# Kernel optimization log

Measured on AMD Instinct MI355X. Metric: run time of the kernel, lower is better.

The kernel has to match this reference:

```python
import jax, jax.numpy as jnp
import numpy as np

B, L, D, H = 4, 2048, 1024, 16
DH = D // H  # 64
MASK_VALUE = -1000000.0
EPS = 1e-12


def setup_inputs() -> dict:
    key = jax.random.key(0)
    ks = jax.random.split(key, 7)
    s = 1.0 / np.sqrt(D)
    x = jax.random.normal(ks[0], (B, L, D), dtype=jnp.float32)
    Wq = jax.random.uniform(ks[1], (D, H * DH), jnp.float32, -s, s)
    Wk = jax.random.uniform(ks[2], (D, H * DH), jnp.float32, -s, s)
    Wv = jax.random.uniform(ks[3], (D, H * DH), jnp.float32, -s, s)
    Wo = jax.random.uniform(ks[4], (H * DH, D), jnp.float32, -s, s)
    gamma = jnp.ones((D,), jnp.float32)
    beta = jnp.zeros((D,), jnp.float32)
    # causal mask: True positions are masked (query m cannot attend to key n > m)
    attn_mask = jnp.triu(jnp.ones((L, L), dtype=bool), k=1)
    return {"x": x, "Wq": Wq, "Wk": Wk, "Wv": Wv, "Wo": Wo,
            "gamma": gamma, "beta": beta, "attn_mask": attn_mask}


def _layernorm(y, gamma, beta):
    mu = jnp.mean(y, axis=-1, keepdims=True)
    var = jnp.mean(jnp.square(y - mu), axis=-1, keepdims=True)
    return (y - mu) * jax.lax.rsqrt(var + EPS) * gamma + beta


def reference(x, Wq, Wk, Wv, Wo, gamma, beta, attn_mask):
    scale = 1.0 / np.sqrt(DH)
    # projections, reshape to heads: B L (H D) -> B H L D
    q = (x @ Wq).reshape(B, L, H, DH).transpose(0, 2, 1, 3)
    k = (x @ Wk).reshape(B, L, H, DH).transpose(0, 2, 1, 3)
    v = (x @ Wv).reshape(B, L, H, DH).transpose(0, 2, 1, 3)
    scores = jnp.einsum('bhmd,bhnd->bhmn', q, k) * scale
    scores = jnp.where(attn_mask, MASK_VALUE, scores)
    probs = jax.nn.softmax(scores, axis=-1)
    z = jnp.einsum('bhmn,bhnd->bhmd', probs, v)
    z = z.transpose(0, 2, 1, 3).reshape(B, L, H * DH)
    out = jax.nn.relu(z @ Wo)
    return _layernorm(out + x, gamma, beta)
```

## Files before the change

kernel.cpp:

```cpp
#include <hip/hip_runtime.h>
#include <math.h>

#define B_ 4
#define L_ 2048
#define D_ 1024
#define H_ 16
#define DH_ 64
#define QKV_N 3072

typedef unsigned short ushort_t;
typedef unsigned int uint_t;
using bf16x8 = __attribute__((ext_vector_type(8))) short;
using f32x4  = __attribute__((ext_vector_type(4))) float;

__device__ __forceinline__ ushort_t f2bf(float f) {
    union { float f; unsigned int u; } v; v.f = f;
    unsigned int u = v.u;
    unsigned int rnd = ((u >> 16) & 1u) + 0x7fffu;
    return (ushort_t)((u + rnd) >> 16);
}

__device__ __forceinline__ float bf2f(ushort_t u) {
    union { unsigned int u; float f; } v;
    v.u = ((unsigned int)u) << 16;
    return v.f;
}

__device__ __forceinline__ void glds16(const void* g, void* l) {
    __builtin_amdgcn_global_load_lds(
        (const __attribute__((address_space(1))) unsigned int*)g,
        (__attribute__((address_space(3))) unsigned int*)l, 16, 0, 0);
}

__global__ __launch_bounds__(256) void prep(const float* __restrict__ Wq,
                                            const float* __restrict__ Wk,
                                            const float* __restrict__ Wv,
                                            const float* __restrict__ Wo,
                                            const float* __restrict__ x,
                                            ushort_t* __restrict__ wcat,
                                            ushort_t* __restrict__ wto,
                                            ushort_t* __restrict__ xb) {
    const int t = threadIdx.x;
    if (blockIdx.z == 4) {
        const int bid = blockIdx.y * 16 + blockIdx.x;
        const int base = bid * 32768 + t * 4;
        #pragma unroll
        for (int it = 0; it < 32; ++it) {
            float4 v = *(const float4*)(x + base + it * 1024);
            ushort4 o;
            o.x = f2bf(v.x); o.y = f2bf(v.y); o.z = f2bf(v.z); o.w = f2bf(v.w);
            *(ushort4*)(xb + base + it * 1024) = o;
        }
        return;
    }
    __shared__ ushort_t tile[64][65];
    const int widx = blockIdx.z;
    const float* W = (widx == 0) ? Wq : (widx == 1) ? Wk : (widx == 2) ? Wv : Wo;
    ushort_t* dst = (widx < 3) ? (wcat + (size_t)widx * 1024 * 1024) : wto;
    const int j = t & 63, i0 = t >> 6;
    const int kbase = blockIdx.y * 64, nbase = blockIdx.x * 64;
    #pragma unroll
    for (int it = 0; it < 16; ++it) {
        int i = it * 4 + i0;
        tile[i][j] = f2bf(W[(size_t)(kbase + i) * 1024 + nbase + j]);
    }
    __syncthreads();
    #pragma unroll
    for (int it = 0; it < 16; ++it) {
        int nn = it * 4 + i0;
        dst[(size_t)(nbase + nn) * 1024 + kbase + j] = tile[j][nn];
    }
}

__global__ __launch_bounds__(512) void gemm8p(const ushort_t* __restrict__ A,
                                              const ushort_t* __restrict__ Wt,
                                              ushort_t* __restrict__ Cbf,
                                              const ushort_t* __restrict__ resid,
                                              ushort_t* __restrict__ vt,
                                              int M, int N, int K, int fuse) {
    __shared__ ushort_t lds[49152];
    const int t = threadIdx.x;
    const int w = t >> 6, ln = t & 63;
    const int l15 = ln & 15, quad = ln >> 4;
    const int wrow = w >> 1, wcol = w & 1;

    int bx = blockIdx.x, by = blockIdx.y;
    {
        int nwg = gridDim.x * gridDim.y;
        if ((nwg & 7) == 0) {
            int flat = by * gridDim.x + bx;
            int nid = (flat & 7) * (nwg >> 3) + (flat >> 3);
            by = nid / gridDim.x;
            bx = nid - by * gridDim.x;
        }
    }
    const int bm = by * 256, bn = bx * 128;

    const ushort_t* Agp[2];
    const ushort_t* Bgp;
    #pragma unroll
    for (int j = 0; j < 2; ++j) {
        int r = j * 128 + (t >> 2);
        int c = (t & 3) ^ ((r >> 1) & 3);
        Agp[j] = A + (size_t)(bm + r) * K + c * 8;
    }
    {
        int r = t >> 2;
        int c = (t & 3) ^ ((r >> 1) & 3);
        Bgp = Wt + (size_t)(bn + r) * K + c * 8;
    }

    const int swz8 = (quad ^ ((l15 >> 1) & 3)) * 8;
    int aoff[4], boff[4];
    #pragma unroll
    for (int mf = 0; mf < 4; ++mf)
        aoff[mf] = (wrow * 64 + mf * 16 + l15) * 32 + swz8;
    #pragma unroll
    for (int nf = 0; nf < 4; ++nf)
        boff[nf] = (wcol * 64 + nf * 16 + l15) * 32 + swz8;

    f32x4 acc[4][4] = {};
    const int NT = K >> 6;

#define ABASE(BUF, KH) ((BUF) * 24576 + (KH) * 12288)
#define BBASE(BUF, KH) (ABASE(BUF, KH) + 8192)

#define STAGE(BUF, KH, KT) do {                                             \
        glds16(Agp[0] + (KT) * 64 + (KH) * 32, &lds[ABASE(BUF, KH) + t * 8]);\
        glds16(Agp[1] + (KT) * 64 + (KH) * 32,                              \
               &lds[ABASE(BUF, KH) + 4096 + t * 8]);                        \
        glds16(Bgp + (KT) * 64 + (KH) * 32, &lds[BBASE(BUF, KH) + t * 8]);  \
    } while (0)

#define VM6 asm volatile("s_waitcnt vmcnt(6)" ::: "memory")
#define VM3 asm volatile("s_waitcnt vmcnt(3)" ::: "memory")
#define VM0 asm volatile("s_waitcnt vmcnt(0)" ::: "memory")
#define NOVM ((void)0)

#define PHASE(BUF, KH, STAGEC, VMW) do {                                    \
        bf16x8 af_[4], bf_[4];                                              \
        _Pragma("unroll")                                                   \
        for (int m_ = 0; m_ < 4; ++m_)                                      \
            af_[m_] = *(const bf16x8*)&lds[ABASE(BUF, KH) + aoff[m_]];      \
        _Pragma("unroll")                                                   \
        for (int n_ = 0; n_ < 4; ++n_)                                      \
            bf_[n_] = *(const bf16x8*)&lds[BBASE(BUF, KH) + boff[n_]];      \
        STAGEC;                                                             \
        VMW;                                                                \
        __builtin_amdgcn_s_barrier();                                       \
        asm volatile("s_waitcnt lgkmcnt(0)" ::: "memory");                  \
        __builtin_amdgcn_s_setprio(1);                                      \
        _Pragma("unroll")                                                   \
        for (int m_ = 0; m_ < 4; ++m_)                                      \
            _Pragma("unroll")                                               \
            for (int n_ = 0; n_ < 4; ++n_)                                  \
                acc[m_][n_] = __builtin_amdgcn_mfma_f32_16x16x32_bf16(      \
                    af_[m_], bf_[n_], acc[m_][n_], 0, 0, 0);                \
        __builtin_amdgcn_s_setprio(0);                                      \
        __builtin_amdgcn_s_barrier();                                       \
    } while (0)

    STAGE(0, 0, 0);
    STAGE(0, 1, 0);
    STAGE(1, 0, 1);
    VM6;
    __builtin_amdgcn_s_barrier();

    for (int it = 0; it < (NT >> 1) - 1; ++it) {
        const int kt1 = 2 * it + 1, kt2 = 2 * it + 2, kt3 = 2 * it + 3;
        PHASE(0, 0, STAGE(1, 1, kt1), VM6);
        PHASE(0, 1, STAGE(0, 0, kt2), VM6);
        PHASE(1, 0, STAGE(0, 1, kt2), VM6);
        PHASE(1, 1, STAGE(1, 0, kt3), VM6);
    }

    PHASE(0, 0, STAGE(1, 1, NT - 1), VM6);
    PHASE(0, 1, NOVM, VM3);
    PHASE(1, 0, NOVM, VM0);
    PHASE(1, 1, NOVM, NOVM);

#undef PHASE
#undef STAGE
#undef ABASE
#undef BBASE

    if (vt && bn >= 2048) {
        #pragma unroll
        for (int mf = 0; mf < 4; ++mf) {
            #pragma unroll
            for (int nf = 0; nf < 4; ++nf) {
                #pragma unroll
                for (int reg = 0; reg < 4; ++reg) {
                    int row = bm + wrow * 64 + mf * 16 + quad * 4 + reg;
                    int col = bn + wcol * 64 + nf * 16 + l15 - 2048;
                    int bb = row >> 11, tok = row & 2047;
                    int h = col >> 6, d = col & 63;
                    int tg = tok & 63;
                    int sc = (tg & 15) * 4 + (tg >> 4);
                    size_t addr = ((size_t)((bb * 16 + h) * 64 + d) << 11)
                                + (tok & ~63) + sc;
                    vt[addr] = f2bf(acc[mf][nf][reg]);
                }
            }
        }
    } else {
        #pragma unroll
        for (int mf = 0; mf < 4; ++mf) {
            #pragma unroll
            for (int nf = 0; nf < 4; ++nf) {
                #pragma unroll
                for (int reg = 0; reg < 4; ++reg) {
                    int row = bm + wrow * 64 + mf * 16 + quad * 4 + reg;
                    int col = bn + wcol * 64 + nf * 16 + l15;
                    size_t idx = (size_t)row * N + col;
                    float v = acc[mf][nf][reg];
                    if (fuse) v = fmaxf(v, 0.f) + bf2f(resid[idx]);
                    Cbf[idx] = f2bf(v);
                }
            }
        }
    }
}

__global__ __launch_bounds__(256) void gemm_mfma(const ushort_t* __restrict__ A,
                                                 const ushort_t* __restrict__ Wt,
                                                 ushort_t* __restrict__ Cbf,
                                                 const ushort_t* __restrict__ resid,
                                                 ushort_t* __restrict__ vt,
                                                 int M, int N, int K, int fuse) {
    __shared__ ushort_t As[128 * 64];
    __shared__ ushort_t Bs[128 * 64];
    const int t = threadIdx.x;
    const int w = t >> 6, ln = t & 63;
    const int l15 = ln & 15, quad = ln >> 4;
    const int bm = blockIdx.y * 128, bn = blockIdx.x * 128;
    const int wm = (w & 1) * 64, wn = (w >> 1) * 64;

    const ushort_t* Ap[4];
    const ushort_t* Bp[4];
    #pragma unroll
    for (int j = 0; j < 4; ++j) {
        const int i = t + j * 256;
        const int r = i >> 3;
        const int qg = (i & 7) ^ (r & 7);
        Ap[j] = A  + (size_t)(bm + r) * K + qg * 8;
        Bp[j] = Wt + (size_t)(bn + r) * K + qg * 8;
    }

    f32x4 acc[4][4] = {};

    for (int k0 = 0; k0 < K; k0 += 64) {
        __syncthreads();
        #pragma unroll
        for (int j = 0; j < 4; ++j) {
            glds16(Ap[j] + k0, &As[(t + j * 256) * 8]);
            glds16(Bp[j] + k0, &Bs[(t + j * 256) * 8]);
        }
        __syncthreads();

        #pragma unroll
        for (int kw = 0; kw < 2; ++kw) {
            bf16x8 af[4], bfr[4];
            #pragma unroll
            for (int im = 0; im < 4; ++im) {
                int row = wm + im * 16 + l15;
                int phys = (kw * 4 + quad) ^ (row & 7);
                af[im] = *(const bf16x8*)&As[row * 64 + phys * 8];
            }
            #pragma unroll
            for (int in = 0; in < 4; ++in) {
                int row = wn + in * 16 + l15;
                int phys = (kw * 4 + quad) ^ (row & 7);
                bfr[in] = *(const bf16x8*)&Bs[row * 64 + phys * 8];
            }
            #pragma unroll
            for (int im = 0; im < 4; ++im)
                #pragma unroll
                for (int in = 0; in < 4; ++in)
                    acc[im][in] = __builtin_amdgcn_mfma_f32_16x16x32_bf16(
                        af[im], bfr[in], acc[im][in], 0, 0, 0);
        }
    }

    if (vt && bn >= 2048) {
        #pragma unroll
        for (int im = 0; im < 4; ++im) {
            #pragma unroll
            for (int in = 0; in < 4; ++in) {
                #pragma unroll
                for (int reg = 0; reg < 4; ++reg) {
                    int row = bm + wm + im * 16 + quad * 4 + reg;
                    int col = bn + wn + in * 16 + l15 - 2048;
                    int bb = row >> 11, tok = row & 2047;
                    int h = col >> 6, d = col & 63;
                    int tg = tok & 63;
                    int sc = (tg & 15) * 4 + (tg >> 4);
                    size_t addr = ((size_t)((bb * 16 + h) * 64 + d) << 11)
                                + (tok & ~63) + sc;
                    vt[addr] = f2bf(acc[im][in][reg]);
                }
            }
        }
    } else {
        #pragma unroll
        for (int im = 0; im < 4; ++im) {
            #pragma unroll
            for (int in = 0; in < 4; ++in) {
                #pragma unroll
                for (int reg = 0; reg < 4; ++reg) {
                    int row = bm + wm + im * 16 + quad * 4 + reg;
                    int col = bn + wn + in * 16 + l15;
                    size_t idx = (size_t)row * N + col;
                    float v = acc[im][in][reg];
                    if (fuse) v = fmaxf(v, 0.f) + bf2f(resid[idx]);
                    Cbf[idx] = f2bf(v);
                }
            }
        }
    }
}

__global__ __launch_bounds__(256) void attn_mfma(const ushort_t* __restrict__ qkv,
                                                 const ushort_t* __restrict__ Vt,
                                                 ushort_t* __restrict__ Zb) {
    __shared__ ushort_t Ks[128 * 64];
    __shared__ ushort_t Vs[64 * 128];
    __shared__ ushort_t Ps[4][32 * 72];
    const int t = threadIdx.x, w = t >> 6, ln = t & 63;
    const int l15 = ln & 15, quad = ln >> 4;
    const int bh = blockIdx.x;
    const int b = bh >> 4, h = bh & 15;
    const int Qt = 15 - blockIdx.y;

    bf16x8 ones;
    #pragma unroll
    for (int i = 0; i < 8; ++i) ones[i] = (short)0x3f80;

    int kkey[4], kq[4], vd[4], vcq[4];
    #pragma unroll
    for (int j = 0; j < 4; ++j) {
        int i = t + j * 256;
        kkey[j] = i >> 3;
        kq[j]   = (i & 7) ^ (kkey[j] & 7);
        vd[j]   = i >> 4;
        int cqp = i & 15;
        vcq[j]  = (cqp & 8) | ((cqp & 7) ^ (vd[j] & 7));
    }
    const ushort_t* Kgb = qkv + 1024 + (size_t)b * L_ * QKV_N + h * DH_;
    const ushort_t* Vgb = Vt + (size_t)((b * H_ + h) * DH_) * L_;

    bf16x8 qf[2][2];
    #pragma unroll
    for (int mt = 0; mt < 2; ++mt) {
        const ushort_t* qrow =
            qkv + (size_t)(b * L_ + Qt * 128 + w * 32 + mt * 16 + l15) * QKV_N + h * DH_;
        qf[mt][0] = *(const bf16x8*)(qrow + quad * 8);
        qf[mt][1] = *(const bf16x8*)(qrow + 32 + quad * 8);
    }

    f32x4 acc_o[2][4] = {};
    f32x4 l_acc[2] = {};

    const float c2 = 0.18033688f;

    for (int kt = 0; kt <= Qt; ++kt) {
        __syncthreads();
        #pragma unroll
        for (int j = 0; j < 4; ++j) {
            glds16(Kgb + (size_t)(kt * 128 + kkey[j]) * QKV_N + kq[j] * 8,
                   &Ks[(t + j * 256) * 8]);
            glds16(Vgb + (size_t)vd[j] * L_ + kt * 128 + vcq[j] * 8,
                   &Vs[(t + j * 256) * 8]);
        }
        __syncthreads();

        const bool masked = (kt == Qt);

        #pragma unroll
        for (int ph = 0; ph < 2; ++ph) {
            if (masked && ph && w < 2) continue;

            f32x4 acc_s[2][4] = {};
            __builtin_amdgcn_s_setprio(1);
            #pragma unroll
            for (int in = 0; in < 4; ++in) {
                const int key = ph * 64 + in * 16 + l15;
                #pragma unroll
                for (int ks = 0; ks < 2; ++ks) {
                    int phys = (ks * 4 + quad) ^ (key & 7);
                    bf16x8 kf = *(const bf16x8*)&Ks[key * 64 + phys * 8];
                    acc_s[0][in] = __builtin_amdgcn_mfma_f32_16x16x32_bf16(
                        qf[0][ks], kf, acc_s[0][in], 0, 0, 0);
                    acc_s[1][in] = __builtin_amdgcn_mfma_f32_16x16x32_bf16(
                        qf[1][ks], kf, acc_s[1][in], 0, 0, 0);
                }
            }
            __builtin_amdgcn_s_setprio(0);

            #pragma unroll
            for (int mt = 0; mt < 2; ++mt) {
                #pragma unroll
                for (int reg = 0; reg < 4; ++reg) {
                    const int row = mt * 16 + quad * 4 + reg;
                    float pv[4];
                    #pragma unroll
                    for (int in = 0; in < 4; ++in) {
                        float s2 = fmaf(acc_s[mt][in][reg], c2, -2.0f);
                        if (masked) {
                            int col = kt * 128 + ph * 64 + in * 16 + l15;
                            int qg  = Qt * 128 + w * 32 + row;
                            s2 = (col > qg) ? -100000.0f : s2;
                        }
                        pv[in] = __builtin_amdgcn_exp2f(s2);
                    }
                    uint_t u01 = __builtin_amdgcn_perm(
                        __float_as_uint(pv[1]), __float_as_uint(pv[0]), 0x07060302u);
                    uint_t u23 = __builtin_amdgcn_perm(
                        __float_as_uint(pv[3]), __float_as_uint(pv[2]), 0x07060302u);
                    uint2* dst = (uint2*)&Ps[w][row * 72 + l15 * 4];
                    *dst = make_uint2(u01, u23);
                }
            }

            __builtin_amdgcn_s_setprio(1);
            #pragma unroll
            for (int ks = 0; ks < 2; ++ks) {
                bf16x8 pf0 = *(const bf16x8*)&Ps[w][(l15) * 72 + ks * 32 + quad * 8];
                bf16x8 pf1 = *(const bf16x8*)&Ps[w][(16 + l15) * 72 + ks * 32 + quad * 8];
                #pragma unroll
                for (int in = 0; in < 4; ++in) {
                    const int d = in * 16 + l15;
                    int physv = ph * 8 + (((ks * 4 + quad) ^ (d & 7)));
                    bf16x8 vf = *(const bf16x8*)&Vs[d * 128 + physv * 8];
                    acc_o[0][in] = __builtin_amdgcn_mfma_f32_16x16x32_bf16(
                        vf, pf0, acc_o[0][in], 0, 0, 0);
                    acc_o[1][in] = __builtin_amdgcn_mfma_f32_16x16x32_bf16(
                        vf, pf1, acc_o[1][in], 0, 0, 0);
                }
                l_acc[0] = __builtin_amdgcn_mfma_f32_16x16x32_bf16(ones, pf0, l_acc[0], 0, 0, 0);
                l_acc[1] = __builtin_amdgcn_mfma_f32_16x16x32_bf16(ones, pf1, l_acc[1], 0, 0, 0);
            }
            __builtin_amdgcn_s_setprio(0);
        }
    }

    #pragma unroll
    for (int mt = 0; mt < 2; ++mt) {
        const float inv = 1.0f / l_acc[mt][0];
        const int row = b * L_ + Qt * 128 + w * 32 + mt * 16 + l15;
        #pragma unroll
        for (int in = 0; in < 4; ++in) {
            const int dbase = h * DH_ + in * 16 + quad * 4;
            f32x4 a = acc_o[mt][in];
            ushort4 o;
            o.x = f2bf(a[0] * inv); o.y = f2bf(a[1] * inv);
            o.z = f2bf(a[2] * inv); o.w = f2bf(a[3] * inv);
            *(ushort4*)(Zb + (size_t)row * D_ + dbase) = o;
        }
    }
}

__global__ __launch_bounds__(256) void ln_kernel(const ushort_t* __restrict__ Y,
                                                 const float* __restrict__ gamma,
                                                 const float* __restrict__ beta,
                                                 float* __restrict__ out) {
    const int row = blockIdx.x * 4 + (threadIdx.x >> 6);
    const int t = threadIdx.x & 63;
    const ushort_t* y = Y + (size_t)row * D_;

    float v[16];
    #pragma unroll
    for (int s = 0; s < 4; ++s) {
        ushort4 u = *(const ushort4*)(y + s * 256 + t * 4);
        v[s * 4 + 0] = bf2f(u.x);
        v[s * 4 + 1] = bf2f(u.y);
        v[s * 4 + 2] = bf2f(u.z);
        v[s * 4 + 3] = bf2f(u.w);
    }

    float sum = 0.f;
    #pragma unroll
    for (int i = 0; i < 16; ++i) sum += v[i];
    #pragma unroll
    for (int k = 1; k < 64; k <<= 1) sum += __shfl_xor(sum, k, 64);
    const float mu = sum * (1.f / (float)D_);

    float var = 0.f;
    #pragma unroll
    for (int i = 0; i < 16; ++i) {
        float d = v[i] - mu;
        var += d * d;
    }
    #pragma unroll
    for (int k = 1; k < 64; k <<= 1) var += __shfl_xor(var, k, 64);
    const float rstd = rsqrtf(var * (1.f / (float)D_) + 1e-12f);

    #pragma unroll
    for (int s = 0; s < 4; ++s) {
        const int col = s * 256 + t * 4;
        float4 g  = *(const float4*)(gamma + col);
        float4 bb = *(const float4*)(beta + col);
        float4 o;
        o.x = (v[s * 4 + 0] - mu) * rstd * g.x + bb.x;
        o.y = (v[s * 4 + 1] - mu) * rstd * g.y + bb.y;
        o.z = (v[s * 4 + 2] - mu) * rstd * g.z + bb.z;
        o.w = (v[s * 4 + 3] - mu) * rstd * g.w + bb.w;
        *(float4*)(out + (size_t)row * D_ + col) = o;
    }
}

extern "C" void kernel_launch(void* const* d_in, const int* in_sizes, int n_in,
                              void* d_out, int out_size, void* d_ws, size_t ws_size,
                              hipStream_t stream) {
    const float* x     = (const float*)d_in[0];
    const float* Wq    = (const float*)d_in[1];
    const float* Wk    = (const float*)d_in[2];
    const float* Wv    = (const float*)d_in[3];
    const float* Wo    = (const float*)d_in[4];
    const float* gamma = (const float*)d_in[5];
    const float* beta  = (const float*)d_in[6];
    float* out = (float*)d_out;

    char* ws = (char*)d_ws;
    ushort_t* x_bf = (ushort_t*)(ws);
    ushort_t* wcat = (ushort_t*)(ws + (16u  << 20));
    ushort_t* wto  = (ushort_t*)(ws + (22u  << 20));
    ushort_t* qkv  = (ushort_t*)(ws + (24u  << 20));
    ushort_t* vt   = (ushort_t*)(ws + (72u  << 20));
    ushort_t* z_bf = (ushort_t*)(ws + (88u  << 20));
    ushort_t* y_bf = (ushort_t*)(ws + (104u << 20));

    const int M = B_ * L_;

    prep<<<dim3(16, 16, 5), 256, 0, stream>>>(Wq, Wk, Wv, Wo, x, wcat, wto, x_bf);

    gemm8p<<<dim3(QKV_N / 128, M / 256), 512, 0, stream>>>(
        x_bf, wcat, qkv, nullptr, vt, M, QKV_N, D_, 0);

    attn_mfma<<<dim3(B_ * H_, 16), 256, 0, stream>>>(qkv, vt, z_bf);

    gemm_mfma<<<dim3(D_ / 128, M / 128), 256, 0, stream>>>(
        z_bf, wto, y_bf, x_bf, nullptr, M, D_, D_, 1);

    ln_kernel<<<M / 4, 256, 0, stream>>>(y_bf, gamma, beta, out);
}
```

Measured before the change: 281.4 us.

## Double-buffer K/V tiles in attention with 64-key stages to overlap loads

Attention now stages K and V in two 64-key LDS buffers instead of one 128-key buffer. The loads for the next tile are issued before computing on the current one, so global-to-LDS latency can overlap the MFMA work. Each iteration needs one barrier instead of two. The trade-off is twice as many iterations and barriers per query tile, and it relies on glds16 completion being covered by the end-of-iteration sync.

```diff
diff --git a/kernel.cpp b/kernel.cpp
--- a/kernel.cpp
+++ b/kernel.cpp
@@ -323,8 +323,8 @@
 __global__ __launch_bounds__(256) void attn_mfma(const ushort_t* __restrict__ qkv,
                                                  const ushort_t* __restrict__ Vt,
                                                  ushort_t* __restrict__ Zb) {
-    __shared__ ushort_t Ks[128 * 64];
-    __shared__ ushort_t Vs[64 * 128];
+    __shared__ ushort_t Ks[2][64 * 64];
+    __shared__ ushort_t Vs[2][64 * 64];
     __shared__ ushort_t Ps[4][32 * 72];
     const int t = threadIdx.x, w = t >> 6, ln = t & 63;
     const int l15 = ln & 15, quad = ln >> 4;
@@ -336,15 +336,12 @@
     #pragma unroll
     for (int i = 0; i < 8; ++i) ones[i] = (short)0x3f80;
 
-    int kkey[4], kq[4], vd[4], vcq[4];
-    #pragma unroll
-    for (int j = 0; j < 4; ++j) {
+    int sr[2], sc[2];
+    #pragma unroll
+    for (int j = 0; j < 2; ++j) {
         int i = t + j * 256;
-        kkey[j] = i >> 3;
-        kq[j]   = (i & 7) ^ (kkey[j] & 7);
-        vd[j]   = i >> 4;
-        int cqp = i & 15;
-        vcq[j]  = (cqp & 8) | ((cqp & 7) ^ (vd[j] & 7));
+        sr[j] = i >> 3;
+        sc[j] = (i & 7) ^ (sr[j] & 7);
     }
     const ushort_t* Kgb = qkv + 1024 + (size_t)b * L_ * QKV_N + h * DH_;
     const ushort_t* Vgb = Vt + (size_t)((b * H_ + h) * DH_) * L_;
@@ -363,32 +360,37 @@
 
     const float c2 = 0.18033688f;
 
-    for (int kt = 0; kt <= Qt; ++kt) {
-        __syncthreads();
-        #pragma unroll
-        for (int j = 0; j < 4; ++j) {
-            glds16(Kgb + (size_t)(kt * 128 + kkey[j]) * QKV_N + kq[j] * 8,
-                   &Ks[(t + j * 256) * 8]);
-            glds16(Vgb + (size_t)vd[j] * L_ + kt * 128 + vcq[j] * 8,
-                   &Vs[(t + j * 256) * 8]);
-        }
-        __syncthreads();
-
-        const bool masked = (kt == Qt);
-
-        #pragma unroll
-        for (int ph = 0; ph < 2; ++ph) {
-            if (masked && ph && w < 2) continue;
-
+#define ASTAGE(BUF, KK) do {                                                \
+        glds16(Kgb + (size_t)((KK) * 64 + sr[0]) * QKV_N + sc[0] * 8,       \
+               &Ks[BUF][t * 8]);                                            \
+        glds16(Kgb + (size_t)((KK) * 64 + sr[1]) * QKV_N + sc[1] * 8,       \
+               &Ks[BUF][(t + 256) * 8]);                                    \
+        glds16(Vgb + (size_t)sr[0] * L_ + (KK) * 64 + sc[0] * 8,            \
+               &Vs[BUF][t * 8]);                                            \
+        glds16(Vgb + (size_t)sr[1] * L_ + (KK) * 64 + sc[1] * 8,            \
+               &Vs[BUF][(t + 256) * 8]);                                    \
+    } while (0)
+
+    const int last = 2 * Qt + 1;
+
+    ASTAGE(0, 0);
+    __syncthreads();
+
+    for (int kk = 0; kk <= last; ++kk) {
+        const int cur = kk & 1;
+        if (kk < last) ASTAGE(cur ^ 1, kk + 1);
+
+        const bool maskedTile = (kk >= 2 * Qt);
+        if (!(kk == last && w < 2)) {
             f32x4 acc_s[2][4] = {};
             __builtin_amdgcn_s_setprio(1);
             #pragma unroll
             for (int in = 0; in < 4; ++in) {
-                const int key = ph * 64 + in * 16 + l15;
+                const int key = in * 16 + l15;
                 #pragma unroll
                 for (int ks = 0; ks < 2; ++ks) {
                     int phys = (ks * 4 + quad) ^ (key & 7);
-                    bf16x8 kf = *(const bf16x8*)&Ks[key * 64 + phys * 8];
+                    bf16x8 kf = *(const bf16x8*)&Ks[cur][key * 64 + phys * 8];
                     acc_s[0][in] = __builtin_amdgcn_mfma_f32_16x16x32_bf16(
                         qf[0][ks], kf, acc_s[0][in], 0, 0, 0);
                     acc_s[1][in] = __builtin_amdgcn_mfma_f32_16x16x32_bf16(
@@ -406,8 +408,8 @@
                     #pragma unroll
                     for (int in = 0; in < 4; ++in) {
                         float s2 = fmaf(acc_s[mt][in][reg], c2, -2.0f);
-                        if (masked) {
-                            int col = kt * 128 + ph * 64 + in * 16 + l15;
+                        if (maskedTile) {
+                            int col = kk * 64 + in * 16 + l15;
                             int qg  = Qt * 128 + w * 32 + row;
                             s2 = (col > qg) ? -100000.0f : s2;
                         }
@@ -430,8 +432,8 @@
                 #pragma unroll
                 for (int in = 0; in < 4; ++in) {
                     const int d = in * 16 + l15;
-                    int physv = ph * 8 + (((ks * 4 + quad) ^ (d & 7)));
-                    bf16x8 vf = *(const bf16x8*)&Vs[d * 128 + physv * 8];
+                    int physv = (ks * 4 + quad) ^ (d & 7);
+                    bf16x8 vf = *(const bf16x8*)&Vs[cur][d * 64 + physv * 8];
                     acc_o[0][in] = __builtin_amdgcn_mfma_f32_16x16x32_bf16(
                         vf, pf0, acc_o[0][in], 0, 0, 0);
                     acc_o[1][in] = __builtin_amdgcn_mfma_f32_16x16x32_bf16(
@@ -442,7 +444,11 @@
             }
             __builtin_amdgcn_s_setprio(0);
         }
-    }
+
+        __syncthreads();
+    }
+
+#undef ASTAGE
 
     #pragma unroll
     for (int mt = 0; mt < 2; ++mt) {
```

Measured after the change: 287.1 us. 1.02x slower.

## Replace 4-slot GEMM LDS pipeline with 3-slot rotating ring buffer

Applied to the files above, without the earlier changes.

The GEMM k-loop drops from four 32-wide LDS slots (double buffer of two halves) to a three-slot rotating ring, keeping prefetch depth at two stages ahead. Shared memory per block falls from 96KB to 72KB, which may let more workgroups or waves reside per CU. The trade-off is one fewer in-flight stage and runtime slot-pointer rotation instead of compile-time constant LDS offsets, which may add address arithmetic and lose some latency hiding.

```diff
diff --git a/kernel.cpp b/kernel.cpp
--- a/kernel.cpp
+++ b/kernel.cpp
@@ -78,7 +78,7 @@
                                               const ushort_t* __restrict__ resid,
                                               ushort_t* __restrict__ vt,
                                               int M, int N, int K, int fuse) {
-    __shared__ ushort_t lds[49152];
+    __shared__ ushort_t lds[36864];
     const int t = threadIdx.x;
     const int w = t >> 6, ln = t & 63;
     const int l15 = ln & 15, quad = ln >> 4;
@@ -117,34 +117,29 @@
         aoff[mf] = (wrow * 64 + mf * 16 + l15) * 32 + swz8;
     #pragma unroll
     for (int nf = 0; nf < 4; ++nf)
-        boff[nf] = (wcol * 64 + nf * 16 + l15) * 32 + swz8;
+        boff[nf] = 8192 + (wcol * 64 + nf * 16 + l15) * 32 + swz8;
 
     f32x4 acc[4][4] = {};
-    const int NT = K >> 6;
-
-#define ABASE(BUF, KH) ((BUF) * 24576 + (KH) * 12288)
-#define BBASE(BUF, KH) (ABASE(BUF, KH) + 8192)
-
-#define STAGE(BUF, KH, KT) do {                                             \
-        glds16(Agp[0] + (KT) * 64 + (KH) * 32, &lds[ABASE(BUF, KH) + t * 8]);\
-        glds16(Agp[1] + (KT) * 64 + (KH) * 32,                              \
-               &lds[ABASE(BUF, KH) + 4096 + t * 8]);                        \
-        glds16(Bgp + (KT) * 64 + (KH) * 32, &lds[BBASE(BUF, KH) + t * 8]);  \
+    const int NS = K >> 5;
+
+#define STAGE(BASE, S) do {                                                 \
+        glds16(Agp[0] + (S) * 32, &lds[(BASE) + t * 8]);                    \
+        glds16(Agp[1] + (S) * 32, &lds[(BASE) + 4096 + t * 8]);             \
+        glds16(Bgp + (S) * 32,    &lds[(BASE) + 8192 + t * 8]);             \
     } while (0)
 
-#define VM6 asm volatile("s_waitcnt vmcnt(6)" ::: "memory")
 #define VM3 asm volatile("s_waitcnt vmcnt(3)" ::: "memory")
 #define VM0 asm volatile("s_waitcnt vmcnt(0)" ::: "memory")
 #define NOVM ((void)0)
 
-#define PHASE(BUF, KH, STAGEC, VMW) do {                                    \
+#define PHASE(RBASE, STAGEC, VMW) do {                                      \
         bf16x8 af_[4], bf_[4];                                              \
         _Pragma("unroll")                                                   \
         for (int m_ = 0; m_ < 4; ++m_)                                      \
-            af_[m_] = *(const bf16x8*)&lds[ABASE(BUF, KH) + aoff[m_]];      \
+            af_[m_] = *(const bf16x8*)&lds[(RBASE) + aoff[m_]];             \
         _Pragma("unroll")                                                   \
         for (int n_ = 0; n_ < 4; ++n_)                                      \
-            bf_[n_] = *(const bf16x8*)&lds[BBASE(BUF, KH) + boff[n_]];      \
+            bf_[n_] = *(const bf16x8*)&lds[(RBASE) + boff[n_]];             \
         STAGEC;                                                             \
         VMW;                                                                \
         __builtin_amdgcn_s_barrier();                                       \
@@ -160,29 +155,21 @@
         __builtin_amdgcn_s_barrier();                                       \
     } while (0)
 
-    STAGE(0, 0, 0);
-    STAGE(0, 1, 0);
-    STAGE(1, 0, 1);
-    VM6;
+    STAGE(0, 0);
+    STAGE(12288, 1);
+    VM3;
     __builtin_amdgcn_s_barrier();
 
-    for (int it = 0; it < (NT >> 1) - 1; ++it) {
-        const int kt1 = 2 * it + 1, kt2 = 2 * it + 2, kt3 = 2 * it + 3;
-        PHASE(0, 0, STAGE(1, 1, kt1), VM6);
-        PHASE(0, 1, STAGE(0, 0, kt2), VM6);
-        PHASE(1, 0, STAGE(0, 1, kt2), VM6);
-        PHASE(1, 1, STAGE(1, 0, kt3), VM6);
-    }
-
-    PHASE(0, 0, STAGE(1, 1, NT - 1), VM6);
-    PHASE(0, 1, NOVM, VM3);
-    PHASE(1, 0, NOVM, VM0);
-    PHASE(1, 1, NOVM, NOVM);
+    int r0 = 0, r1 = 12288, r2 = 24576;
+    for (int s = 0; s < NS - 2; ++s) {
+        PHASE(r0, STAGE(r2, s + 2), VM3);
+        int tmp = r0; r0 = r1; r1 = r2; r2 = tmp;
+    }
+    PHASE(r0, NOVM, VM0);
+    PHASE(r1, NOVM, NOVM);
 
 #undef PHASE
 #undef STAGE
-#undef ABASE
-#undef BBASE
 
     if (vt && bn >= 2048) {
         #pragma unroll
```

New measurement: 275.7 us (median of 2 runs). -2.0%, faster.
